# Kernel optimization log

Measured on AMD Instinct MI355X. Metric: run time of the kernel, lower is better.

The kernel has to match this reference:

```python
import jax, jax.numpy as jnp
import numpy as np

N, E = 50000, 800000
C, A_ALL, RAD_IN, FC1, FC2 = 128, 256, 32, 64, 64
H, AH, VH = 8, 16, 16  # heads, alpha channels/head, value channels/head


def _radial_mlp(x, w1, b1, w2, b2, w3, b3):
    x = jax.nn.silu(x @ w1 + b1)
    x = jax.nn.silu(x @ w2 + b2)
    return x @ w3 + b3


def _smooth_leaky_relu(x, a=0.2):
    # Equiformer SmoothLeakyReLU: 0.5*(1+a)*x + 0.5*(1-a)*x*(2*sigmoid(x)-1)
    return 0.5 * (1.0 + a) * x + 0.5 * (1.0 - a) * x * (2.0 * jax.nn.sigmoid(x) - 1.0)


def _segment_softmax(scores, seg, num_segments):
    m = jax.ops.segment_max(scores, seg, num_segments=num_segments)
    m = jnp.where(jnp.isfinite(m), m, 0.0)
    e = jnp.exp(scores - m[seg])
    s = jax.ops.segment_sum(e, seg, num_segments=num_segments)
    return e / (s[seg] + 1e-16)


def setup_inputs():
    key = jax.random.key(0)
    ks = jax.random.split(key, 16)

    def g(k, shape):
        scale = 1.0 / np.sqrt(shape[0])
        return jax.random.normal(k, shape, dtype=jnp.float32) * scale

    return {
        "node_input": jax.random.normal(ks[0], (N, C), dtype=jnp.float32),
        "node_attr": jnp.ones((N, 1), jnp.float32),
        "edge_attr": jax.random.uniform(ks[1], (E, 1), dtype=jnp.float32),
        "edge_scalars": jax.random.normal(ks[2], (E, RAD_IN), dtype=jnp.float32),
        "edge_src": jax.random.randint(ks[3], (E,), 0, N, dtype=jnp.int32),
        "edge_dst": jax.random.randint(ks[4], (E,), 0, N, dtype=jnp.int32),
        "batch": jnp.zeros((N,), jnp.int32),
        "w_src": g(ks[5], (C, C)), "b_src": jnp.zeros((C,), jnp.float32),
        "w_dst": g(ks[6], (C, C)),
        "fc_w1": g(ks[7], (RAD_IN, FC1)), "fc_b1": jnp.zeros((FC1,), jnp.float32),
        "fc_w2": g(ks[8], (FC1, FC2)), "fc_b2": jnp.zeros((FC2,), jnp.float32),
        "fc_w3": g(ks[9], (FC2, C)), "fc_b3": jnp.zeros((C,), jnp.float32),
        "w_sep": g(ks[10], (C, A_ALL)), "b_sep": jnp.zeros((A_ALL,), jnp.float32),
        "alpha_dot": jax.random.normal(ks[11], (1, H, AH), dtype=jnp.float32) * np.sqrt(2.0 / (H * AH)),
        "w_proj": g(ks[12], (H * VH, C)), "b_proj": jnp.zeros((C,), jnp.float32),
    }


def reference(node_input, node_attr, edge_attr, edge_scalars, edge_src, edge_dst, batch,
              w_src, b_src, w_dst, fc_w1, fc_b1, fc_w2, fc_b2, fc_w3, fc_b3,
              w_sep, b_sep, alpha_dot, w_proj, b_proj):
    n_nodes = node_input.shape[0]
    n_edges = edge_src.shape[0]
    # merge_src / merge_dst (LinearRS; bias only on src)
    msg_src = node_input @ w_src + b_src                     # [N, C]
    msg_dst = node_input @ w_dst                             # [N, C]
    message = msg_src[edge_src] + msg_dst[edge_dst]          # [E, C] edge gather
    # SeparableFCTP: radial-weighted depthwise tensor product (scalar irreps)
    rad_w = _radial_mlp(edge_scalars, fc_w1, fc_b1, fc_w2, fc_b2, fc_w3, fc_b3)  # [E, C]
    message = message * edge_attr * rad_w                    # depthwise TP
    message = message @ w_sep + b_sep                        # [E, A_ALL] linear to attn_all
    # Vec2AttnHeads + split alpha/value per head
    msg_h = message.reshape(n_edges, H, AH + VH)
    alpha = _smooth_leaky_relu(msg_h[:, :, :AH])             # [E, H, AH]
    value = msg_h[:, :, AH:]                                 # [E, H, VH]
    score = jnp.einsum('ehk,ahk->eh', alpha, alpha_dot)      # [E, H]
    att = _segment_softmax(score, edge_dst, n_nodes)[..., None]
    out = jax.ops.segment_sum(value * att, edge_dst, num_segments=n_nodes)  # scatter-add
    out = out.reshape(n_nodes, H * VH)                       # AttnHeads2Vec
    return out @ w_proj + b_proj
```

## Files before the change

### kernel.cpp

```cpp
#include <hip/hip_runtime.h>

#define NN 50000
#define NE 800000

typedef unsigned short u16;
typedef __bf16 bf16x8 __attribute__((ext_vector_type(8)));
typedef float f32x4 __attribute__((ext_vector_type(4)));
typedef unsigned short u16x8 __attribute__((ext_vector_type(8)));

__device__ __forceinline__ u16 f2b(float f){
  return __builtin_bit_cast(u16, (__bf16)f);
}
__device__ __forceinline__ float b2f(u16 b){
  return __uint_as_float(((unsigned)b)<<16);
}
__device__ __forceinline__ float row_sum16(float x){
  x += __int_as_float(__builtin_amdgcn_update_dpp(0, __float_as_int(x), 0x121, 0xF, 0xF, true));
  x += __int_as_float(__builtin_amdgcn_update_dpp(0, __float_as_int(x), 0x122, 0xF, 0xF, true));
  x += __int_as_float(__builtin_amdgcn_update_dpp(0, __float_as_int(x), 0x124, 0xF, 0xF, true));
  x += __int_as_float(__builtin_amdgcn_update_dpp(0, __float_as_int(x), 0x128, 0xF, 0xF, true));
  return x;
}
#define MFMA16(a,b,c) __builtin_amdgcn_mfma_f32_16x16x32_bf16((a),(b),(c),0,0,0)

__global__ void k_prep(const float* __restrict__ w1, const float* __restrict__ w2,
                       const float* __restrict__ w3, const float* __restrict__ wsep,
                       const float* __restrict__ wsrc, const float* __restrict__ wdst,
                       const float* __restrict__ wproj,
                       u16* __restrict__ w1T, u16* __restrict__ w2T,
                       u16* __restrict__ w3T, u16* __restrict__ wsepT,
                       u16* __restrict__ wsrcT, u16* __restrict__ wdstT,
                       u16* __restrict__ wprojT)
{
  int id = blockIdx.x*256 + threadIdx.x;
  if (id < 2048)  { int n=id>>5,  k=id&31;  w1T[id]   = f2b(w1[k*64+n]);    return; } id -= 2048;
  if (id < 4096)  { int n=id>>6,  k=id&63;  w2T[id]   = f2b(w2[k*64+n]);    return; } id -= 4096;
  if (id < 8192)  { int n=id>>6,  k=id&63;  w3T[id]   = f2b(w3[k*128+n]);   return; } id -= 8192;
  if (id < 32768) { int n=id>>7,  k=id&127; wsepT[id] = f2b(wsep[k*256+n]); return; } id -= 32768;
  if (id < 16384) { int n=id>>7,  k=id&127; wsrcT[id] = f2b(wsrc[k*128+n]); return; } id -= 16384;
  if (id < 16384) { int n=id>>7,  k=id&127; wdstT[id] = f2b(wdst[k*128+n]); return; } id -= 16384;
  if (id < 16384) { int n=id>>7,  k=id&127; wprojT[id]= f2b(wproj[k*128+n]); return; }
}

__global__ void k_hist(const int* __restrict__ edst, unsigned* __restrict__ cnt)
{
  int e = blockIdx.x*256 + threadIdx.x;
  if (e < NE) atomicAdd(&cnt[edst[e]], 1u);
}

__launch_bounds__(1024)
__global__ void k_scan(const unsigned* __restrict__ cnt, unsigned* __restrict__ cur)
{
  __shared__ unsigned sWt[16];
  __shared__ unsigned sCarry;
  const int tid = threadIdx.x, lane = tid&63, w = tid>>6;
  if (tid == 0) sCarry = 0u;
  __syncthreads();
  for (int base = 0; base < NN; base += 1024){
    int i = base + tid;
    unsigned v = (i < NN) ? cnt[i] : 0u;
    unsigned x = v;
    #pragma unroll
    for (int off=1; off<64; off<<=1){
      unsigned t = __shfl_up(x, off);
      if (lane >= off) x += t;
    }
    if (lane == 63) sWt[w] = x;
    __syncthreads();
    unsigned wOff = 0;
    for (int k=0;k<16;++k) if (k < w) wOff += sWt[k];
    if (i < NN) cur[i] = sCarry + wOff + (x - v);
    __syncthreads();
    if (tid == 1023) sCarry += wOff + x;
    __syncthreads();
  }
}

__global__ void k_scatter(const int* __restrict__ esrc, const int* __restrict__ edst,
                          const float* __restrict__ eattr, unsigned* __restrict__ cur,
                          int4* __restrict__ ework)
{
  int e = blockIdx.x*256 + threadIdx.x;
  if (e < NE){
    int d = edst[e];
    unsigned pos = atomicAdd(&cur[d], 1u);
    ework[pos] = make_int4(e, d, esrc[e], __float_as_int(eattr[e]));
  }
}

__launch_bounds__(256)
__global__ void k_node(const float* __restrict__ x, const u16* __restrict__ wsrcT,
                       const u16* __restrict__ wdstT, const float* __restrict__ bsrc,
                       u16* __restrict__ msgsrcB, u16* __restrict__ msgdstB)
{
  __shared__ u16 sX[64*136];
  __shared__ u16 sW[128*136];
  __shared__ float sB[128];
  const int tid = threadIdx.x;
  const int n0 = blockIdx.x*64;
  for (int idx = tid; idx < 64*32; idx += 256){
    int r = idx>>5, s = idx&31;
    float4 v = make_float4(0.f,0.f,0.f,0.f);
    if (n0 + r < NN) v = *(const float4*)(x + (size_t)(n0+r)*128 + s*4);
    ushort4 o; o.x=f2b(v.x); o.y=f2b(v.y); o.z=f2b(v.z); o.w=f2b(v.w);
    *(ushort4*)(&sX[r*136 + s*4]) = o;
  }
  const int wave = tid>>6, lane = tid&63, l15 = lane&15, q = lane>>4;
  for (int half = 0; half < 2; ++half){
    const u16* wT = half ? wdstT : wsrcT;
    for (int idx = tid; idx < 128*16; idx += 256){
      int r = idx>>4, s = idx&15;
      *(uint4*)(&sW[r*136 + s*8]) = *(const uint4*)(wT + r*128 + s*8);
    }
    if (tid < 128) sB[tid] = half ? 0.0f : bsrc[tid];
    __syncthreads();
    f32x4 acc[8];
    #pragma unroll
    for (int n=0;n<8;++n) acc[n] = (f32x4){0.f,0.f,0.f,0.f};
    #pragma unroll
    for (int k0=0;k0<128;k0+=32){
      bf16x8 a = *(const bf16x8*)(&sX[(wave*16+l15)*136 + k0 + q*8]);
      #pragma unroll
      for (int n=0;n<8;++n){
        bf16x8 b = *(const bf16x8*)(&sW[(n*16+l15)*136 + k0 + q*8]);
        acc[n] = MFMA16(a,b,acc[n]);
      }
    }
    u16* outp = half ? msgdstB : msgsrcB;
    #pragma unroll
    for (int n=0;n<8;++n){
      #pragma unroll
      for (int r=0;r<4;++r){
        int row = n0 + wave*16 + q*4 + r;
        if (row < NN) outp[(size_t)row*128 + n*16 + l15] = f2b(acc[n][r] + sB[n*16+l15]);
      }
    }
    __syncthreads();
  }
}

#define PM 136
#define PH 72
#define PX 40
__launch_bounds__(256,6)
__global__ void k_edge(const float* __restrict__ escal, const int4* __restrict__ ework,
                       const u16* __restrict__ msgsrcB, const u16* __restrict__ msgdstB,
                       const u16* __restrict__ w1T, const u16* __restrict__ w2T,
                       const u16* __restrict__ w3T, const u16* __restrict__ wsepT,
                       const float* __restrict__ b1, const float* __restrict__ b2,
                       const float* __restrict__ b3, const float* __restrict__ bsep,
                       const float* __restrict__ adot,
                       float* __restrict__ num, float* __restrict__ denom)
{
  __shared__ __attribute__((aligned(16))) char pool[26624];
  u16* sH1  = (u16*)(pool + 0);
  u16* sXs  = (u16*)(pool + 9216);
  u16* sH2  = (u16*)(pool + 17408);
  u16* sMsg = (u16*)(pool + 0);

  const int tid = threadIdx.x;
  const int e0 = blockIdx.x*64;
  const int wave = tid>>6, lane = tid&63, l15 = lane&15, q = lane>>4;

  for (int j = tid; j < 512; j += 256){ int r=j>>3, s=j&7;
    int pe = ework[e0 + r].x;
    float4 v = *(const float4*)(escal + (size_t)pe*32 + s*4);
    ushort4 o; o.x=f2b(v.x); o.y=f2b(v.y); o.z=f2b(v.z); o.w=f2b(v.w);
    *(ushort4*)&sXs[r*PX + s*4] = o; }
  __syncthreads();

  {
    f32x4 acc[4];
    #pragma unroll
    for (int n=0;n<4;++n) acc[n] = (f32x4){0.f,0.f,0.f,0.f};
    bf16x8 a = *(const bf16x8*)&sXs[(wave*16+l15)*PX + q*8];
    #pragma unroll
    for (int n=0;n<4;++n){
      bf16x8 b = *(const bf16x8*)(w1T + (n*16+l15)*32 + q*8);
      acc[n] = MFMA16(a,b,acc[n]);
    }
    #pragma unroll
    for (int n=0;n<4;++n){
      float bia = b1[n*16+l15];
      #pragma unroll
      for (int r=0;r<4;++r){
        float v = acc[n][r] + bia;
        float h = v / (1.0f + __expf(-v));
        sH1[(wave*16+q*4+r)*PH + n*16+l15] = f2b(h);
      }
    }
  }
  __syncthreads();

  {
    f32x4 acc[4];
    #pragma unroll
    for (int n=0;n<4;++n) acc[n] = (f32x4){0.f,0.f,0.f,0.f};
    #pragma unroll
    for (int k0=0;k0<64;k0+=32){
      bf16x8 a = *(const bf16x8*)&sH1[(wave*16+l15)*PH + k0 + q*8];
      #pragma unroll
      for (int n=0;n<4;++n){
        bf16x8 b = *(const bf16x8*)(w2T + (n*16+l15)*64 + k0 + q*8);
        acc[n] = MFMA16(a,b,acc[n]);
      }
    }
    #pragma unroll
    for (int n=0;n<4;++n){
      float bia = b2[n*16+l15];
      #pragma unroll
      for (int r=0;r<4;++r){
        float v = acc[n][r] + bia;
        float h = v / (1.0f + __expf(-v));
        sH2[(wave*16+q*4+r)*PH + n*16+l15] = f2b(h);
      }
    }
  }
  __syncthreads();

  {
    const int m0 = (wave&1)*2, n0 = (wave>>1)*2;
    #pragma unroll
    for (int ch=0; ch<2; ++ch){
      f32x4 acc[2][2];
      #pragma unroll
      for (int mm=0;mm<2;++mm)
        #pragma unroll
        for (int nn=0;nn<2;++nn) acc[mm][nn] = (f32x4){0.f,0.f,0.f,0.f};
      const u16* w3b = w3T + (size_t)(ch*64)*64;
      #pragma unroll
      for (int k0=0;k0<64;k0+=32){
        bf16x8 a0 = *(const bf16x8*)&sH2[((m0  )*16+l15)*PH + k0 + q*8];
        bf16x8 a1 = *(const bf16x8*)&sH2[((m0+1)*16+l15)*PH + k0 + q*8];
        bf16x8 bb0 = *(const bf16x8*)(w3b + ((n0  )*16+l15)*64 + k0 + q*8);
        bf16x8 bb1 = *(const bf16x8*)(w3b + ((n0+1)*16+l15)*64 + k0 + q*8);
        acc[0][0] = MFMA16(a0,bb0,acc[0][0]);
        acc[1][0] = MFMA16(a1,bb0,acc[1][0]);
        acc[0][1] = MFMA16(a0,bb1,acc[0][1]);
        acc[1][1] = MFMA16(a1,bb1,acc[1][1]);
      }
      #pragma unroll
      for (int mm=0;mm<2;++mm){
        #pragma unroll
        for (int nn=0;nn<2;++nn){
          int c = ch*64 + (n0+nn)*16 + l15;
          float bia = b3[c];
          #pragma unroll
          for (int r=0;r<4;++r){
            float v = acc[mm][nn][r] + bia;
            sMsg[((m0+mm)*16+q*4+r)*PM + c] = f2b(v);
          }
        }
      }
    }
  }
  __syncthreads();

  for (int idx = tid; idx < 64*16; idx += 256){
    int r = idx>>4, s = idx&15;
    int cs = s*8;
    int4 em = ework[e0 + r];
    int id = em.y, is = em.z;
    float ea = __int_as_float(em.w);
    u16x8 a8 = *(const u16x8*)(msgsrcB + (size_t)is*128 + cs);
    u16x8 d8 = *(const u16x8*)(msgdstB + (size_t)id*128 + cs);
    u16x8 rw = *(const u16x8*)&sMsg[r*PM + cs];
    u16x8 o;
    #pragma unroll
    for (int j=0;j<8;++j){
      o[j] = f2b((b2f(a8[j]) + b2f(d8[j])) * ea * b2f(rw[j]));
    }
    *(u16x8*)&sMsg[r*PM + cs] = o;
  }
  __syncthreads();

  {
    const int fm0 = (wave&1)*2, fn0 = (wave>>1)*2;
    const int hh = fn0>>1;
    float* sWV = (float*)(pool + 17408);
    float* sWp = (float*)(pool + 17408 + 8704);
    const u16* wb0 = wsepT + (size_t)((fn0  )*16+l15)*128 + q*8;
    const u16* wb1 = wsepT + (size_t)((fn0+1)*16+l15)*128 + q*8;
    const int wc = tid & 31, wg = tid >> 5, wcl = wc & 15, whh = wc >> 4;
    int dreg[8];
    #pragma unroll
    for (int rr=0; rr<8; ++rr) dreg[rr] = ework[e0 + wg*8 + rr].y;

    #pragma unroll
    for (int ch=0; ch<4; ++ch){
      f32x4 acc[2][2];
      #pragma unroll
      for (int mm=0;mm<2;++mm)
        #pragma unroll
        for (int nn=0;nn<2;++nn) acc[mm][nn] = (f32x4){0.f,0.f,0.f,0.f};
      #pragma unroll
      for (int k0=0;k0<128;k0+=32){
        bf16x8 a0 = *(const bf16x8*)&sMsg[((fm0  )*16+l15)*PM + k0 + q*8];
        bf16x8 a1 = *(const bf16x8*)&sMsg[((fm0+1)*16+l15)*PM + k0 + q*8];
        bf16x8 bb0 = *(const bf16x8*)(wb0 + (size_t)ch*64*128 + k0);
        bf16x8 bb1 = *(const bf16x8*)(wb1 + (size_t)ch*64*128 + k0);
        acc[0][0] = MFMA16(a0,bb0,acc[0][0]);
        acc[1][0] = MFMA16(a1,bb0,acc[1][0]);
        acc[0][1] = MFMA16(a0,bb1,acc[0][1]);
        acc[1][1] = MFMA16(a1,bb1,acc[1][1]);
      }
      {
        const int h  = ch*2 + hh;
        const int ca = ch*64 + fn0*16;
        const float ba = bsep[ca + l15];
        const float bv = bsep[ca + 16 + l15];
        const float ad = adot[h*16 + l15];
        #pragma unroll
        for (int mm=0;mm<2;++mm){
          #pragma unroll
          for (int r=0;r<4;++r){
            float av  = acc[mm][0][r] + ba;
            float sig = 1.0f/(1.0f + __expf(-av));
            float sl  = av*(0.2f + 0.8f*sig);
            float contrib = row_sum16(sl * ad);
            float w  = __expf(contrib);
            float vv = acc[mm][1][r] + bv;
            int row  = (fm0+mm)*16 + q*4 + r;
            sWV[row*34 + hh*16 + l15] = w*vv;
            if (l15 == 0) sWp[row*2 + hh] = w;
          }
        }
      }
      __syncthreads();
      {
        const int h = ch*2 + whh;
        float av = 0.f, wa = 0.f;
        int pd = dreg[0];
        #pragma unroll
        for (int rr=0; rr<8; ++rr){
          int d = dreg[rr];
          if (d != pd){
            unsafeAtomicAdd(&num[(size_t)pd*128 + h*16 + wcl], av);
            if (wcl == 0) unsafeAtomicAdd(&denom[(size_t)pd*8 + h], wa);
            av = 0.f; wa = 0.f; pd = d;
          }
          int row = wg*8 + rr;
          av += sWV[row*34 + wc];
          if (wcl == 0) wa += sWp[row*2 + whh];
        }
        unsafeAtomicAdd(&num[(size_t)pd*128 + h*16 + wcl], av);
        if (wcl == 0) unsafeAtomicAdd(&denom[(size_t)pd*8 + h], wa);
      }
      __syncthreads();
    }
  }
}

__launch_bounds__(256)
__global__ void k_out(const float* __restrict__ num, const float* __restrict__ denom,
                      const u16* __restrict__ wprojT, const float* __restrict__ bproj,
                      float* __restrict__ out)
{
  __shared__ u16 sX[64*136];
  __shared__ u16 sW[128*136];
  __shared__ float sB[128];
  const int tid = threadIdx.x;
  const int n0 = blockIdx.x*64;
  for (int idx = tid; idx < 64*128; idx += 256){
    int r = idx>>7, c = idx&127;
    float xv = 0.f;
    int row = n0 + r;
    if (row < NN){
      float d = denom[row*8 + (c>>4)];
      xv = num[(size_t)row*128 + c] / (d + 1e-16f);
    }
    sX[r*136 + c] = f2b(xv);
  }
  for (int idx = tid; idx < 128*16; idx += 256){ int r=idx>>4, s=idx&15;
    *(uint4*)&sW[r*136 + s*8] = *(const uint4*)(wprojT + r*128 + s*8); }
  if (tid < 128) sB[tid] = bproj[tid];
  __syncthreads();
  const int wave = tid>>6, lane = tid&63, l15 = lane&15, q = lane>>4;
  f32x4 acc[8];
  #pragma unroll
  for (int n=0;n<8;++n) acc[n] = (f32x4){0.f,0.f,0.f,0.f};
  #pragma unroll
  for (int k0=0;k0<128;k0+=32){
    bf16x8 a = *(const bf16x8*)&sX[(wave*16+l15)*136 + k0 + q*8];
    #pragma unroll
    for (int n=0;n<8;++n){
      bf16x8 b = *(const bf16x8*)&sW[(n*16+l15)*136 + k0 + q*8];
      acc[n] = MFMA16(a,b,acc[n]);
    }
  }
  #pragma unroll
  for (int n=0;n<8;++n){
    #pragma unroll
    for (int r=0;r<4;++r){
      int row = n0 + wave*16 + q*4 + r;
      if (row < NN) out[(size_t)row*128 + n*16 + l15] = acc[n][r] + sB[n*16+l15];
    }
  }
}

extern "C" void kernel_launch(void* const* d_in, const int* in_sizes, int n_in,
                              void* d_out, int out_size, void* d_ws, size_t ws_size,
                              hipStream_t stream)
{
  const float* node_input = (const float*)d_in[0];
  const float* eattr = (const float*)d_in[2];
  const float* escal = (const float*)d_in[3];
  const int*   esrc  = (const int*)d_in[4];
  const int*   edst  = (const int*)d_in[5];
  const float* wsrc  = (const float*)d_in[7];
  const float* bsrc  = (const float*)d_in[8];
  const float* wdst  = (const float*)d_in[9];
  const float* w1    = (const float*)d_in[10];
  const float* b1    = (const float*)d_in[11];
  const float* w2    = (const float*)d_in[12];
  const float* b2    = (const float*)d_in[13];
  const float* w3    = (const float*)d_in[14];
  const float* b3    = (const float*)d_in[15];
  const float* wsep  = (const float*)d_in[16];
  const float* bsep  = (const float*)d_in[17];
  const float* adot  = (const float*)d_in[18];
  const float* wproj = (const float*)d_in[19];
  const float* bproj = (const float*)d_in[20];

  char* ws = (char*)d_ws;
  size_t off = 0;
  auto alloc = [&](size_t bytes)->void*{ void* p = ws + off; off += (bytes + 255) & ~(size_t)255; return p; };
  u16*   msgsrcB = (u16*)alloc((size_t)NN*128*2);
  u16*   msgdstB = (u16*)alloc((size_t)NN*128*2);
  float* num     = (float*)alloc((size_t)NN*128*4);
  float* denom   = (float*)alloc((size_t)NN*8*4);
  u16* w1T    = (u16*)alloc(2048*2);
  u16* w2T    = (u16*)alloc(4096*2);
  u16* w3T    = (u16*)alloc(8192*2);
  u16* wsepT  = (u16*)alloc(32768*2);
  u16* wsrcT  = (u16*)alloc(16384*2);
  u16* wdstT  = (u16*)alloc(16384*2);
  u16* wprojT = (u16*)alloc(16384*2);
  unsigned* cnt = (unsigned*)alloc((size_t)NN*4);
  unsigned* cur = (unsigned*)alloc((size_t)NN*4);
  int4*  ework  = (int4*)alloc((size_t)NE*16);

  hipMemsetAsync(num,   0, (size_t)NN*128*4, stream);
  hipMemsetAsync(denom, 0, (size_t)NN*8*4,   stream);
  hipMemsetAsync(cnt,   0, (size_t)NN*4,     stream);

  k_prep<<<376, 256, 0, stream>>>(w1,w2,w3,wsep,wsrc,wdst,wproj,
                                  w1T,w2T,w3T,wsepT,wsrcT,wdstT,wprojT);
  k_hist<<<3125, 256, 0, stream>>>(edst, cnt);
  k_scan<<<1, 1024, 0, stream>>>(cnt, cur);
  k_scatter<<<3125, 256, 0, stream>>>(esrc, edst, eattr, cur, ework);
  k_node<<<782, 256, 0, stream>>>(node_input, wsrcT, wdstT, bsrc, msgsrcB, msgdstB);
  k_edge<<<12500, 256, 0, stream>>>(escal, ework, msgsrcB, msgdstB,
                                    w1T, w2T, w3T, wsepT, b1, b2, b3, bsep, adot,
                                    num, denom);
  k_out<<<782, 256, 0, stream>>>(num, denom, wprojT, bproj, (float*)d_out);
}
```

Measured before the change: 800.8 us.

## Parallelize prefix scan across blocks and trim edge-kernel syncs and LDS reloads

Replaces the single-block serial scan over node counts with a three-kernel multi-block scan (block-local scan, block-totals scan, add offsets). In the edge kernel, each wave now loads only its own 16 rows of edge scalars, which lets two __syncthreads be dropped. The A fragments for the attention projection are hoisted out of the chunk loop so they are read from LDS once rather than four times. The cost is two extra kernel launches and more registers held for the hoisted fragments.

```diff
diff --git a/kernel.cpp b/kernel.cpp
--- a/kernel.cpp
+++ b/kernel.cpp
@@ -49,31 +49,54 @@
 }
 
 __launch_bounds__(1024)
-__global__ void k_scan(const unsigned* __restrict__ cnt, unsigned* __restrict__ cur)
-{
-  __shared__ unsigned sWt[16];
-  __shared__ unsigned sCarry;
+__global__ void k_scan1(const unsigned* __restrict__ cnt, unsigned* __restrict__ cur,
+                        unsigned* __restrict__ btot)
+{
+  __shared__ unsigned wt[16];
   const int tid = threadIdx.x, lane = tid&63, w = tid>>6;
-  if (tid == 0) sCarry = 0u;
-  __syncthreads();
-  for (int base = 0; base < NN; base += 1024){
-    int i = base + tid;
-    unsigned v = (i < NN) ? cnt[i] : 0u;
-    unsigned x = v;
-    #pragma unroll
-    for (int off=1; off<64; off<<=1){
-      unsigned t = __shfl_up(x, off);
-      if (lane >= off) x += t;
-    }
-    if (lane == 63) sWt[w] = x;
-    __syncthreads();
-    unsigned wOff = 0;
-    for (int k=0;k<16;++k) if (k < w) wOff += sWt[k];
-    if (i < NN) cur[i] = sCarry + wOff + (x - v);
-    __syncthreads();
-    if (tid == 1023) sCarry += wOff + x;
-    __syncthreads();
-  }
+  int i = blockIdx.x*1024 + tid;
+  unsigned v = (i < NN) ? cnt[i] : 0u;
+  unsigned x = v;
+  #pragma unroll
+  for (int off=1; off<64; off<<=1){
+    unsigned t = __shfl_up(x, off);
+    if (lane >= off) x += t;
+  }
+  if (lane == 63) wt[w] = x;
+  __syncthreads();
+  if (w == 0){
+    unsigned y = (lane < 16) ? wt[lane] : 0u;
+    #pragma unroll
+    for (int off=1; off<16; off<<=1){
+      unsigned t = __shfl_up(y, off);
+      if (lane >= off) y += t;
+    }
+    if (lane < 16) wt[lane] = y;
+  }
+  __syncthreads();
+  unsigned wo = w ? wt[w-1] : 0u;
+  if (i < NN) cur[i] = wo + (x - v);
+  if (tid == 1023) btot[blockIdx.x] = wo + x;
+}
+
+__global__ void k_scan2(unsigned* __restrict__ btot)
+{
+  int lane = threadIdx.x;
+  unsigned v = (lane < 49) ? btot[lane] : 0u;
+  unsigned x = v;
+  #pragma unroll
+  for (int off=1; off<64; off<<=1){
+    unsigned t = __shfl_up(x, off);
+    if (lane >= off) x += t;
+  }
+  if (lane < 49) btot[lane] = x - v;
+}
+
+__launch_bounds__(1024)
+__global__ void k_scan3(unsigned* __restrict__ cur, const unsigned* __restrict__ btot)
+{
+  int i = blockIdx.x*1024 + threadIdx.x;
+  if (i < NN) cur[i] += btot[blockIdx.x];
 }
 
 __global__ void k_scatter(const int* __restrict__ esrc, const int* __restrict__ edst,
@@ -162,12 +185,19 @@
   const int e0 = blockIdx.x*64;
   const int wave = tid>>6, lane = tid&63, l15 = lane&15, q = lane>>4;
 
-  for (int j = tid; j < 512; j += 256){ int r=j>>3, s=j&7;
-    int pe = ework[e0 + r].x;
-    float4 v = *(const float4*)(escal + (size_t)pe*32 + s*4);
-    ushort4 o; o.x=f2b(v.x); o.y=f2b(v.y); o.z=f2b(v.z); o.w=f2b(v.w);
-    *(ushort4*)&sXs[r*PX + s*4] = o; }
-  __syncthreads();
+  {
+    int row  = wave*16 + (lane>>2);
+    int part = lane&3;
+    int pe = ework[e0 + row].x;
+    const float* srcp = escal + (size_t)pe*32 + part*8;
+    float4 v0 = *(const float4*)(srcp);
+    float4 v1 = *(const float4*)(srcp + 4);
+    ushort4 o0, o1;
+    o0.x=f2b(v0.x); o0.y=f2b(v0.y); o0.z=f2b(v0.z); o0.w=f2b(v0.w);
+    o1.x=f2b(v1.x); o1.y=f2b(v1.y); o1.z=f2b(v1.z); o1.w=f2b(v1.w);
+    *(ushort4*)&sXs[row*PX + part*8]     = o0;
+    *(ushort4*)&sXs[row*PX + part*8 + 4] = o1;
+  }
 
   {
     f32x4 acc[4];
@@ -190,7 +220,6 @@
       }
     }
   }
-  __syncthreads();
 
   {
     f32x4 acc[4];
@@ -286,6 +315,13 @@
     #pragma unroll
     for (int rr=0; rr<8; ++rr) dreg[rr] = ework[e0 + wg*8 + rr].y;
 
+    bf16x8 afr[2][4];
+    #pragma unroll
+    for (int mm=0;mm<2;++mm)
+      #pragma unroll
+      for (int k=0;k<4;++k)
+        afr[mm][k] = *(const bf16x8*)&sMsg[((fm0+mm)*16+l15)*PM + k*32 + q*8];
+
     #pragma unroll
     for (int ch=0; ch<4; ++ch){
       f32x4 acc[2][2];
@@ -294,15 +330,13 @@
         #pragma unroll
         for (int nn=0;nn<2;++nn) acc[mm][nn] = (f32x4){0.f,0.f,0.f,0.f};
       #pragma unroll
-      for (int k0=0;k0<128;k0+=32){
-        bf16x8 a0 = *(const bf16x8*)&sMsg[((fm0  )*16+l15)*PM + k0 + q*8];
-        bf16x8 a1 = *(const bf16x8*)&sMsg[((fm0+1)*16+l15)*PM + k0 + q*8];
-        bf16x8 bb0 = *(const bf16x8*)(wb0 + (size_t)ch*64*128 + k0);
-        bf16x8 bb1 = *(const bf16x8*)(wb1 + (size_t)ch*64*128 + k0);
-        acc[0][0] = MFMA16(a0,bb0,acc[0][0]);
-        acc[1][0] = MFMA16(a1,bb0,acc[1][0]);
-        acc[0][1] = MFMA16(a0,bb1,acc[0][1]);
-        acc[1][1] = MFMA16(a1,bb1,acc[1][1]);
+      for (int k0=0;k0<4;++k0){
+        bf16x8 bb0 = *(const bf16x8*)(wb0 + (size_t)ch*64*128 + k0*32);
+        bf16x8 bb1 = *(const bf16x8*)(wb1 + (size_t)ch*64*128 + k0*32);
+        acc[0][0] = MFMA16(afr[0][k0],bb0,acc[0][0]);
+        acc[1][0] = MFMA16(afr[1][k0],bb0,acc[1][0]);
+        acc[0][1] = MFMA16(afr[0][k0],bb1,acc[0][1]);
+        acc[1][1] = MFMA16(afr[1][k0],bb1,acc[1][1]);
       }
       {
         const int h  = ch*2 + hh;
@@ -438,6 +472,7 @@
   u16* wprojT = (u16*)alloc(16384*2);
   unsigned* cnt = (unsigned*)alloc((size_t)NN*4);
   unsigned* cur = (unsigned*)alloc((size_t)NN*4);
+  unsigned* btot = (unsigned*)alloc(64*4);
   int4*  ework  = (int4*)alloc((size_t)NE*16);
 
   hipMemsetAsync(num,   0, (size_t)NN*128*4, stream);
@@ -447,7 +482,9 @@
   k_prep<<<376, 256, 0, stream>>>(w1,w2,w3,wsep,wsrc,wdst,wproj,
                                   w1T,w2T,w3T,wsepT,wsrcT,wdstT,wprojT);
   k_hist<<<3125, 256, 0, stream>>>(edst, cnt);
-  k_scan<<<1, 1024, 0, stream>>>(cnt, cur);
+  k_scan1<<<49, 1024, 0, stream>>>(cnt, cur, btot);
+  k_scan2<<<1, 64, 0, stream>>>(btot);
+  k_scan3<<<49, 1024, 0, stream>>>(cur, btot);
   k_scatter<<<3125, 256, 0, stream>>>(esrc, edst, eattr, cur, ework);
   k_node<<<782, 256, 0, stream>>>(node_input, wsrcT, wdstT, bsrc, msgsrcB, msgdstB);
   k_edge<<<12500, 256, 0, stream>>>(escal, ework, msgsrcB, msgdstB,
```

Result: slower. 978.1 us (+22.1%).
